# Performance work log

Hardware: AMD Instinct MI355X
Metric: run time of the kernel (lower is better)

Reference implementation:

```python
import jax, jax.numpy as jnp
import numpy as np

D_MODEL = 1024
N_HEADS = 16
HEAD_DIM = D_MODEL // N_HEADS
B, S = 2, 2048


def setup_inputs() -> dict:
    key = jax.random.key(0)
    ks = jax.random.split(key, 12)
    std = 1.0 / np.sqrt(D_MODEL)
    mk = lambda k: (jax.random.normal(k, (D_MODEL, D_MODEL), jnp.float32) * std)
    return {
        "query": jax.random.normal(ks[0], (B, S, D_MODEL), jnp.float32),
        "key": jax.random.normal(ks[1], (B, S, D_MODEL), jnp.float32),
        "value": jax.random.normal(ks[2], (B, S, D_MODEL), jnp.float32),
        "Wq": mk(ks[3]), "bq": jnp.zeros((D_MODEL,), jnp.float32),
        "Wk": mk(ks[4]), "bk": jnp.zeros((D_MODEL,), jnp.float32),
        "Wv": mk(ks[5]), "bv": jnp.zeros((D_MODEL,), jnp.float32),
        "Wo": mk(ks[6]), "bo": jnp.zeros((D_MODEL,), jnp.float32),
    }


def reference(query, key, value, Wq, bq, Wk, bk, Wv, bv, Wo, bo):
    b, s, d = query.shape
    # Linear projections (torch Linear: x @ W.T + b)
    q = query @ Wq.T + bq
    k = key @ Wk.T + bk
    v = value @ Wv.T + bv
    # [B, H, S, Dh]
    split = lambda x: x.reshape(b, -1, N_HEADS, HEAD_DIM).transpose(0, 2, 1, 3)
    qh, kh, vh = split(q), split(k), split(v)
    scores = jnp.einsum("bhqd,bhkd->bhqk", qh, kh) / jnp.sqrt(
        jnp.asarray(HEAD_DIM, qh.dtype))
    attn = jax.nn.softmax(scores, axis=-1)
    out = jnp.einsum("bhqk,bhkd->bhqd", attn, vh)
    out = out.transpose(0, 2, 1, 3).reshape(b, -1, N_HEADS * HEAD_DIM)
    return out @ Wo.T + bo
```

## Files before the change

kernel.cpp:

```cpp
#include <hip/hip_runtime.h>
#include <hip/hip_bf16.h>


typedef short bf16x8 __attribute__((ext_vector_type(8)));
typedef short bf16x4 __attribute__((ext_vector_type(4)));
typedef float f32x4  __attribute__((ext_vector_type(4)));

constexpr size_t NE = (size_t)4096 * 1024;
constexpr size_t NW = (size_t)1024 * 1024;

#if __has_builtin(__builtin_amdgcn_exp2f)
#define EXP2(x) __builtin_amdgcn_exp2f(x)
#else
#define EXP2(x) exp2f(x)
#endif

__device__ __forceinline__ short f2bf(float f) {
  __hip_bfloat16 h = __float2bfloat16(f);
  return *reinterpret_cast<short*>(&h);
}

__device__ __forceinline__ void cp16(const short* g, short* l) {
  __builtin_amdgcn_global_load_lds(
      (const __attribute__((address_space(1))) void*)g,
      (__attribute__((address_space(3))) void*)l, 16, 0, 0);
}

__device__ __forceinline__ int xcd_swz(int x, int nblk) {
  return (x & 7) * (nblk >> 3) + (x >> 3);
}

__global__ __launch_bounds__(256) void cvt_kernel(
    const float* q, const float* k, const float* v,
    const float* Wq, const float* Wk, const float* Wv, const float* Wo,
    short* qb, short* kb, short* vb,
    short* Wqb, short* Wkb, short* Wvb, short* Wob) {
  const int y = blockIdx.y;
  const float* s; short* d;
  if (y < 12) {
    const int t = y >> 2;
    const size_t off = (size_t)(y & 3) << 20;
    s = (t == 0 ? q : (t == 1 ? k : v)) + off;
    d = (t == 0 ? qb : (t == 1 ? kb : vb)) + off;
  } else {
    s = (y == 12 ? Wq : (y == 13 ? Wk : (y == 14 ? Wv : Wo)));
    d = (y == 12 ? Wqb : (y == 13 ? Wkb : (y == 14 ? Wvb : Wob)));
  }
  size_t i = (size_t)blockIdx.x * 256 + threadIdx.x;
  float4 val = ((const float4*)s)[i];
  bf16x4 o;
  o[0] = f2bf(val.x); o[1] = f2bf(val.y); o[2] = f2bf(val.z); o[3] = f2bf(val.w);
  ((bf16x4*)d)[i] = o;
}

__global__ __launch_bounds__(256) void gemm_qkv(
    const short* __restrict__ A0, const short* __restrict__ A1, const short* __restrict__ A2,
    const short* __restrict__ W0, const short* __restrict__ W1, const short* __restrict__ W2,
    const float* __restrict__ b0, const float* __restrict__ b1, const float* __restrict__ b2,
    short* __restrict__ C0, short* __restrict__ C1, short* __restrict__ Cv) {
  __shared__ short As[3][128 * 32];
  __shared__ short Bs[3][128 * 32];
  const int which = blockIdx.y;
  const short* A    = which == 0 ? A0 : (which == 1 ? A1 : A2);
  const short* W    = which == 0 ? W0 : (which == 1 ? W1 : W2);
  const float* bias = which == 0 ? b0 : (which == 1 ? b1 : b2);
  const float scale = which == 0 ? 0.18033688011112042f : 1.0f;

  const int tid  = threadIdx.x;
  const int bx   = xcd_swz((int)blockIdx.x, 256);
  const int bm   = bx >> 3;
  const int bn   = bx & 7;
  const int lane = tid & 63, wid = tid >> 6;
  const int g = lane >> 4, l15 = lane & 15;
  const int wm = (wid >> 1) * 64, wn = (wid & 1) * 64;

  const short* Ag = A + (size_t)(bm * 128 + (tid >> 2)) * 1024 + (tid & 3) * 8;
  const short* Wg = W + (size_t)(bn * 128 + (tid >> 2)) * 1024 + (tid & 3) * 8;
  const int wofs = wid * 512;

#define QKV_STAGE(t, b)                               \
  do {                                                \
    const int kk_ = (t) * 32;                         \
    cp16(Ag + kk_,             As[(b)] + wofs);       \
    cp16(Ag + 64 * 1024 + kk_, As[(b)] + wofs + 2048);\
    cp16(Wg + kk_,             Bs[(b)] + wofs);       \
    cp16(Wg + 64 * 1024 + kk_, Bs[(b)] + wofs + 2048);\
  } while (0)

  f32x4 acc[4][4];
#pragma unroll
  for (int i = 0; i < 4; ++i)
#pragma unroll
    for (int j = 0; j < 4; ++j) acc[i][j] = (f32x4){0.f, 0.f, 0.f, 0.f};

  QKV_STAGE(0, 0);
  QKV_STAGE(1, 1);

  for (int t = 0; t < 32; ++t) {
    const int cur = t % 3;
    if (t < 30) {
      QKV_STAGE(t + 2, (t + 2) % 3);
      asm volatile("s_waitcnt vmcnt(8)" ::: "memory");
    } else if (t == 30) {
      asm volatile("s_waitcnt vmcnt(4)" ::: "memory");
    } else {
      asm volatile("s_waitcnt vmcnt(0)" ::: "memory");
    }
    __builtin_amdgcn_s_barrier();

    bf16x8 af[4], bfr[4];
#pragma unroll
    for (int mt = 0; mt < 4; ++mt)
      af[mt] = *(const bf16x8*)&As[cur][(wm + mt * 16 + l15) * 32 + g * 8];
#pragma unroll
    for (int nt = 0; nt < 4; ++nt)
      bfr[nt] = *(const bf16x8*)&Bs[cur][(wn + nt * 16 + l15) * 32 + g * 8];
#pragma unroll
    for (int mt = 0; mt < 4; ++mt)
#pragma unroll
      for (int nt = 0; nt < 4; ++nt)
        acc[mt][nt] = __builtin_amdgcn_mfma_f32_16x16x32_bf16(
            af[mt], bfr[nt], acc[mt][nt], 0, 0, 0);

    asm volatile("s_waitcnt lgkmcnt(0)" ::: "memory");
    __builtin_amdgcn_s_barrier();
  }
#undef QKV_STAGE

  const int col0 = bn * 128 + wn;
  if (which < 2) {
    short* C = which == 0 ? C0 : C1;
#pragma unroll
    for (int nt = 0; nt < 4; ++nt) {
      const int col = col0 + nt * 16 + l15;
      const float bb = bias[col];
#pragma unroll
      for (int mt = 0; mt < 4; ++mt) {
        const int m0 = bm * 128 + wm + mt * 16 + g * 4;
#pragma unroll
        for (int r = 0; r < 4; ++r)
          C[(size_t)(m0 + r) * 1024 + col] = f2bf((acc[mt][nt][r] + bb) * scale);
      }
    }
  } else {
#pragma unroll
    for (int nt = 0; nt < 4; ++nt) {
      const int col = col0 + nt * 16 + l15;
      const int h = col >> 6, dh = col & 63;
      const float bb = bias[col];
#pragma unroll
      for (int mt = 0; mt < 4; ++mt) {
        const int m0 = bm * 128 + wm + mt * 16 + g * 4;
        const int bb_ = m0 >> 11, s0 = m0 & 2047;
        bf16x4 o;
#pragma unroll
        for (int r = 0; r < 4; ++r) o[r] = f2bf(acc[mt][nt][r] + bb);
        *(bf16x4*)&Cv[(((size_t)bb_ * 16 + h) * 64 + dh) * 2048 + s0] = o;
      }
    }
  }
}

__global__ __launch_bounds__(256) void gemm_out(
    const short* __restrict__ A, const short* __restrict__ W,
    const float* __restrict__ bias, float* __restrict__ C) {
  __shared__ short As[3][64 * 32];
  __shared__ short Bs[3][128 * 32];
  const int tid  = threadIdx.x;
  const int bx   = xcd_swz((int)blockIdx.x, 512);
  const int bm   = bx >> 3;
  const int bn   = bx & 7;
  const int lane = tid & 63, wid = tid >> 6;
  const int g = lane >> 4, l15 = lane & 15;
  const int wm = (wid >> 1) * 32, wn = (wid & 1) * 64;

  const short* Ag = A + (size_t)(bm * 64 + (tid >> 2)) * 1024 + (tid & 3) * 8;
  const short* Wg = W + (size_t)(bn * 128 + (tid >> 2)) * 1024 + (tid & 3) * 8;
  const int wofs = wid * 512;

#define OUT_STAGE(t, b)                               \
  do {                                                \
    const int kk_ = (t) * 32;                         \
    cp16(Ag + kk_,             As[(b)] + wofs);       \
    cp16(Wg + kk_,             Bs[(b)] + wofs);       \
    cp16(Wg + 64 * 1024 + kk_, Bs[(b)] + wofs + 2048);\
  } while (0)

  f32x4 acc[2][4];
#pragma unroll
  for (int i = 0; i < 2; ++i)
#pragma unroll
    for (int j = 0; j < 4; ++j) acc[i][j] = (f32x4){0.f, 0.f, 0.f, 0.f};

  OUT_STAGE(0, 0);
  OUT_STAGE(1, 1);

  for (int t = 0; t < 32; ++t) {
    const int cur = t % 3;
    if (t < 30) {
      OUT_STAGE(t + 2, (t + 2) % 3);
      asm volatile("s_waitcnt vmcnt(6)" ::: "memory");
    } else if (t == 30) {
      asm volatile("s_waitcnt vmcnt(3)" ::: "memory");
    } else {
      asm volatile("s_waitcnt vmcnt(0)" ::: "memory");
    }
    __builtin_amdgcn_s_barrier();

    bf16x8 af[2], bfr[4];
#pragma unroll
    for (int mt = 0; mt < 2; ++mt)
      af[mt] = *(const bf16x8*)&As[cur][(wm + mt * 16 + l15) * 32 + g * 8];
#pragma unroll
    for (int nt = 0; nt < 4; ++nt)
      bfr[nt] = *(const bf16x8*)&Bs[cur][(wn + nt * 16 + l15) * 32 + g * 8];
#pragma unroll
    for (int mt = 0; mt < 2; ++mt)
#pragma unroll
      for (int nt = 0; nt < 4; ++nt)
        acc[mt][nt] = __builtin_amdgcn_mfma_f32_16x16x32_bf16(
            af[mt], bfr[nt], acc[mt][nt], 0, 0, 0);

    asm volatile("s_waitcnt lgkmcnt(0)" ::: "memory");
    __builtin_amdgcn_s_barrier();
  }
#undef OUT_STAGE

  const int col0 = bn * 128 + wn;
#pragma unroll
  for (int nt = 0; nt < 4; ++nt) {
    const int col = col0 + nt * 16 + l15;
    const float bb = bias[col];
#pragma unroll
    for (int mt = 0; mt < 2; ++mt) {
      const int m0 = bm * 64 + wm + mt * 16 + g * 4;
#pragma unroll
      for (int r = 0; r < 4; ++r)
        C[(size_t)(m0 + r) * 1024 + col] = acc[mt][nt][r] + bb;
    }
  }
}

__global__ __launch_bounds__(512) void attn_kernel(
    const short* __restrict__ Q, const short* __restrict__ K,
    const short* __restrict__ Vg, short* __restrict__ O) {
  __shared__ __align__(16) char smem[73728];
  short (*Kt)[64][72] = (short(*)[64][72])smem;
  short (*Vt)[64][72] = (short(*)[64][72])(smem + 18432);
  short (*Pt)[32][72] = (short(*)[32][72])(smem + 36864);
  float* M = (float*)smem;

  const int tid  = threadIdx.x;
  const int bx   = xcd_swz((int)blockIdx.x, 512);
  const int qt   = bx & 15;
  const int bh   = bx >> 4;
  const int b    = bh >> 4, h = bh & 15;
  const int lane = tid & 63, wid = tid >> 6;
  const int par  = wid >> 2;
  const int w4   = wid & 3;
  const int g = lane >> 4, l15 = lane & 15;

  const int q0 = qt * 128 + w4 * 32;
  bf16x8 qf[2][2];
#pragma unroll
  for (int mt = 0; mt < 2; ++mt) {
    const size_t base = (size_t)(b * 2048 + q0 + mt * 16 + l15) * 1024 + h * 64;
    qf[mt][0] = *(const bf16x8*)(Q + base + g * 8);
    qf[mt][1] = *(const bf16x8*)(Q + base + 32 + g * 8);
  }

  f32x4 o_acc[2][4];
#pragma unroll
  for (int i = 0; i < 2; ++i)
#pragma unroll
    for (int j = 0; j < 4; ++j) o_acc[i][j] = (f32x4){0.f, 0.f, 0.f, 0.f};
  float l_i[2][4];
#pragma unroll
  for (int i = 0; i < 2; ++i)
#pragma unroll
    for (int r = 0; r < 4; ++r) l_i[i][r] = 0.f;

  const int st   = tid & 255;
  const int spar = tid >> 8;
  const int srow = st >> 2, sch = st & 3;
  const short* Kbase = K + (size_t)(b * 2048) * 1024 + h * 64 + sch * 8;
  const short* Vbase = Vg + (size_t)((b * 16 + h) * 64 + srow) * 2048 + sch * 8;

  bf16x8 nk0, nk1, nv0, nv1;
  {
    const short* krow = Kbase + (size_t)(spar * 64 + srow) * 1024;
    nk0 = *(const bf16x8*)(krow);
    nk1 = *(const bf16x8*)(krow + 32);
    nv0 = *(const bf16x8*)(Vbase + spar * 64);
    nv1 = *(const bf16x8*)(Vbase + spar * 64 + 32);
  }

  for (int ktp = 0; ktp < 16; ++ktp) {
    __syncthreads();
    *(bf16x8*)&Kt[spar][srow][sch * 8]      = nk0;
    *(bf16x8*)&Kt[spar][srow][sch * 8 + 32] = nk1;
    *(bf16x8*)&Vt[spar][srow][sch * 8]      = nv0;
    *(bf16x8*)&Vt[spar][srow][sch * 8 + 32] = nv1;
    __syncthreads();

    if (ktp < 15) {
      const int kn = (ktp + 1) * 2 + spar;
      const short* krow = Kbase + (size_t)(kn * 64 + srow) * 1024;
      nk0 = *(const bf16x8*)(krow);
      nk1 = *(const bf16x8*)(krow + 32);
      nv0 = *(const bf16x8*)(Vbase + kn * 64);
      nv1 = *(const bf16x8*)(Vbase + kn * 64 + 32);
    }

    f32x4 sv[2][4];
#pragma unroll
    for (int nt = 0; nt < 4; ++nt) {
      bf16x8 kf0 = *(const bf16x8*)&Kt[par][nt * 16 + l15][g * 8];
      bf16x8 kf1 = *(const bf16x8*)&Kt[par][nt * 16 + l15][32 + g * 8];
#pragma unroll
      for (int mt = 0; mt < 2; ++mt) {
        f32x4 z = (f32x4){0.f, 0.f, 0.f, 0.f};
        z = __builtin_amdgcn_mfma_f32_16x16x32_bf16(qf[mt][0], kf0, z, 0, 0, 0);
        z = __builtin_amdgcn_mfma_f32_16x16x32_bf16(qf[mt][1], kf1, z, 0, 0, 0);
        sv[mt][nt] = z;
      }
    }

#pragma unroll
    for (int mt = 0; mt < 2; ++mt)
#pragma unroll
      for (int r = 0; r < 4; ++r) {
        float p0 = EXP2(sv[mt][0][r]);
        float p1 = EXP2(sv[mt][1][r]);
        float p2 = EXP2(sv[mt][2][r]);
        float p3 = EXP2(sv[mt][3][r]);
        l_i[mt][r] += (p0 + p1) + (p2 + p3);
        const int pr = mt * 16 + g * 4 + r;
        Pt[wid][pr][l15]      = f2bf(p0);
        Pt[wid][pr][16 + l15] = f2bf(p1);
        Pt[wid][pr][32 + l15] = f2bf(p2);
        Pt[wid][pr][48 + l15] = f2bf(p3);
      }

    bf16x8 pf[2][2];
#pragma unroll
    for (int mt = 0; mt < 2; ++mt) {
      pf[mt][0] = *(const bf16x8*)&Pt[wid][mt * 16 + l15][g * 8];
      pf[mt][1] = *(const bf16x8*)&Pt[wid][mt * 16 + l15][32 + g * 8];
    }
#pragma unroll
    for (int nt = 0; nt < 4; ++nt) {
      bf16x8 vf0 = *(const bf16x8*)&Vt[par][nt * 16 + l15][g * 8];
      bf16x8 vf1 = *(const bf16x8*)&Vt[par][nt * 16 + l15][32 + g * 8];
#pragma unroll
      for (int mt = 0; mt < 2; ++mt) {
        o_acc[mt][nt] = __builtin_amdgcn_mfma_f32_16x16x32_bf16(
            pf[mt][0], vf0, o_acc[mt][nt], 0, 0, 0);
        o_acc[mt][nt] = __builtin_amdgcn_mfma_f32_16x16x32_bf16(
            pf[mt][1], vf1, o_acc[mt][nt], 0, 0, 0);
      }
    }
  }

  __syncthreads();
  if (par == 1) {
    float* dst = M + (size_t)(w4 * 64 + lane) * 40;
#pragma unroll
    for (int mt = 0; mt < 2; ++mt)
#pragma unroll
      for (int nt = 0; nt < 4; ++nt)
        *(f32x4*)(dst + (mt * 4 + nt) * 4) = o_acc[mt][nt];
#pragma unroll
    for (int mt = 0; mt < 2; ++mt)
#pragma unroll
      for (int r = 0; r < 4; ++r) dst[32 + mt * 4 + r] = l_i[mt][r];
  }
  __syncthreads();
  if (par == 0) {
    const float* src = M + (size_t)(w4 * 64 + lane) * 40;
#pragma unroll
    for (int mt = 0; mt < 2; ++mt)
#pragma unroll
      for (int nt = 0; nt < 4; ++nt)
        o_acc[mt][nt] += *(const f32x4*)(src + (mt * 4 + nt) * 4);
#pragma unroll
    for (int mt = 0; mt < 2; ++mt)
#pragma unroll
      for (int r = 0; r < 4; ++r) l_i[mt][r] += src[32 + mt * 4 + r];

#pragma unroll
    for (int mt = 0; mt < 2; ++mt)
#pragma unroll
      for (int r = 0; r < 4; ++r) {
        float l = l_i[mt][r];
#pragma unroll
        for (int off = 1; off < 16; off <<= 1) l += __shfl_xor(l, off, 64);
        const float inv = 1.0f / l;
        const int row = q0 + mt * 16 + g * 4 + r;
        const size_t base = (size_t)(b * 2048 + row) * 1024 + h * 64;
#pragma unroll
        for (int nt = 0; nt < 4; ++nt)
          O[base + nt * 16 + l15] = f2bf(o_acc[mt][nt][r] * inv);
      }
  }
}

extern "C" void kernel_launch(void* const* d_in, const int* in_sizes, int n_in,
                              void* d_out, int out_size, void* d_ws, size_t ws_size,
                              hipStream_t stream) {
  (void)in_sizes; (void)n_in; (void)out_size; (void)ws_size;
  const float* q  = (const float*)d_in[0];
  const float* k  = (const float*)d_in[1];
  const float* v  = (const float*)d_in[2];
  const float* Wq = (const float*)d_in[3];
  const float* bq = (const float*)d_in[4];
  const float* Wk = (const float*)d_in[5];
  const float* bk = (const float*)d_in[6];
  const float* Wv = (const float*)d_in[7];
  const float* bv = (const float*)d_in[8];
  const float* Wo = (const float*)d_in[9];
  const float* bo = (const float*)d_in[10];
  float* out = (float*)d_out;

  short* qb  = (short*)d_ws;
  short* kb  = qb + NE;
  short* vb  = kb + NE;
  short* Wqb = vb + NE;
  short* Wkb = Wqb + NW;
  short* Wvb = Wkb + NW;
  short* Wob = Wvb + NW;
  short* Qw  = Wob + NW;
  short* Kw  = Qw + NE;
  short* Vtg = Kw + NE;
  short* Ob  = qb;

  cvt_kernel<<<dim3(1024, 16), 256, 0, stream>>>(q, k, v, Wq, Wk, Wv, Wo,
                                                 qb, kb, vb, Wqb, Wkb, Wvb, Wob);
  gemm_qkv<<<dim3(256, 3), 256, 0, stream>>>(qb, kb, vb, Wqb, Wkb, Wvb,
                                             bq, bk, bv, Qw, Kw, Vtg);
  attn_kernel<<<512, 512, 0, stream>>>(Qw, Kw, Vtg, Ob);
  gemm_out<<<512, 256, 0, stream>>>(Ob, Wob, bo, out);
}
```

Measured before the change: 219.1 us.

## Keep attention P in registers via transposed MFMA and permuted V layout

Swaps the MFMA operand order so the score tile comes out transposed (keys along rows), letting the exp'd probabilities be packed directly into the B-operand registers for the PV MFMA instead of round-tripping through LDS. To make this work, the V projection epilogue writes sequence positions in a permuted order within each 64-chunk so the register layout matches. This removes the P LDS buffer, halving shared memory and adding an occupancy hint, and the row-sum and output store become simpler (fewer shuffles, vectorized bf16x4 stores). It relies on the permutation exactly matching the MFMA fragment layout, so any mismatch would silently corrupt results.

New measurement: 321.1 us. 1.47x slower.

```diff
diff --git a/kernel.cpp b/kernel.cpp
--- a/kernel.cpp
+++ b/kernel.cpp
@@ -152,10 +152,13 @@
       for (int mt = 0; mt < 4; ++mt) {
         const int m0 = bm * 128 + wm + mt * 16 + g * 4;
         const int bb_ = m0 >> 11, s0 = m0 & 2047;
+        const int k6 = s0 & 63;
+        const int cpos = (s0 & ~63) | (((k6 >> 4) & 2) << 4)
+                       | (((k6 >> 2) & 3) << 3) | (((k6 >> 4) & 1) << 2);
         bf16x4 o;
 #pragma unroll
         for (int r = 0; r < 4; ++r) o[r] = f2bf(acc[mt][nt][r] + bb);
-        *(bf16x4*)&Cv[(((size_t)bb_ * 16 + h) * 64 + dh) * 2048 + s0] = o;
+        *(bf16x4*)&Cv[(((size_t)bb_ * 16 + h) * 64 + dh) * 2048 + cpos] = o;
       }
     }
   }
@@ -241,13 +244,12 @@
   }
 }
 
-__global__ __launch_bounds__(512) void attn_kernel(
+__global__ __launch_bounds__(512, 6) void attn_kernel(
     const short* __restrict__ Q, const short* __restrict__ K,
     const short* __restrict__ Vg, short* __restrict__ O) {
-  __shared__ __align__(16) char smem[73728];
+  __shared__ __align__(16) char smem[36864];
   short (*Kt)[64][72] = (short(*)[64][72])smem;
   short (*Vt)[64][72] = (short(*)[64][72])(smem + 18432);
-  short (*Pt)[32][72] = (short(*)[32][72])(smem + 36864);
   float* M = (float*)smem;
 
   const int tid  = threadIdx.x;
@@ -274,11 +276,7 @@
   for (int i = 0; i < 2; ++i)
 #pragma unroll
     for (int j = 0; j < 4; ++j) o_acc[i][j] = (f32x4){0.f, 0.f, 0.f, 0.f};
-  float l_i[2][4];
-#pragma unroll
-  for (int i = 0; i < 2; ++i)
-#pragma unroll
-    for (int r = 0; r < 4; ++r) l_i[i][r] = 0.f;
+  float l_i[2] = {0.f, 0.f};
 
   const int st   = tid & 255;
   const int spar = tid >> 8;
@@ -320,34 +318,27 @@
 #pragma unroll
       for (int mt = 0; mt < 2; ++mt) {
         f32x4 z = (f32x4){0.f, 0.f, 0.f, 0.f};
-        z = __builtin_amdgcn_mfma_f32_16x16x32_bf16(qf[mt][0], kf0, z, 0, 0, 0);
-        z = __builtin_amdgcn_mfma_f32_16x16x32_bf16(qf[mt][1], kf1, z, 0, 0, 0);
+        z = __builtin_amdgcn_mfma_f32_16x16x32_bf16(kf0, qf[mt][0], z, 0, 0, 0);
+        z = __builtin_amdgcn_mfma_f32_16x16x32_bf16(kf1, qf[mt][1], z, 0, 0, 0);
         sv[mt][nt] = z;
       }
     }
 
-#pragma unroll
-    for (int mt = 0; mt < 2; ++mt)
-#pragma unroll
-      for (int r = 0; r < 4; ++r) {
-        float p0 = EXP2(sv[mt][0][r]);
-        float p1 = EXP2(sv[mt][1][r]);
-        float p2 = EXP2(sv[mt][2][r]);
-        float p3 = EXP2(sv[mt][3][r]);
-        l_i[mt][r] += (p0 + p1) + (p2 + p3);
-        const int pr = mt * 16 + g * 4 + r;
-        Pt[wid][pr][l15]      = f2bf(p0);
-        Pt[wid][pr][16 + l15] = f2bf(p1);
-        Pt[wid][pr][32 + l15] = f2bf(p2);
-        Pt[wid][pr][48 + l15] = f2bf(p3);
-      }
-
     bf16x8 pf[2][2];
 #pragma unroll
     for (int mt = 0; mt < 2; ++mt) {
-      pf[mt][0] = *(const bf16x8*)&Pt[wid][mt * 16 + l15][g * 8];
-      pf[mt][1] = *(const bf16x8*)&Pt[wid][mt * 16 + l15][32 + g * 8];
-    }
+      float s = 0.f;
+#pragma unroll
+      for (int nt = 0; nt < 4; ++nt)
+#pragma unroll
+        for (int r = 0; r < 4; ++r) {
+          float p = EXP2(sv[mt][nt][r]);
+          s += p;
+          pf[mt][nt >> 1][(nt & 1) * 4 + r] = f2bf(p);
+        }
+      l_i[mt] += s;
+    }
+
 #pragma unroll
     for (int nt = 0; nt < 4; ++nt) {
       bf16x8 vf0 = *(const bf16x8*)&Vt[par][nt * 16 + l15][g * 8];
@@ -355,53 +346,51 @@
 #pragma unroll
       for (int mt = 0; mt < 2; ++mt) {
         o_acc[mt][nt] = __builtin_amdgcn_mfma_f32_16x16x32_bf16(
-            pf[mt][0], vf0, o_acc[mt][nt], 0, 0, 0);
+            vf0, pf[mt][0], o_acc[mt][nt], 0, 0, 0);
         o_acc[mt][nt] = __builtin_amdgcn_mfma_f32_16x16x32_bf16(
-            pf[mt][1], vf1, o_acc[mt][nt], 0, 0, 0);
+            vf1, pf[mt][1], o_acc[mt][nt], 0, 0, 0);
       }
     }
   }
 
   __syncthreads();
   if (par == 1) {
-    float* dst = M + (size_t)(w4 * 64 + lane) * 40;
+    float* dst = M + (size_t)(w4 * 64 + lane) * 36;
 #pragma unroll
     for (int mt = 0; mt < 2; ++mt)
 #pragma unroll
       for (int nt = 0; nt < 4; ++nt)
         *(f32x4*)(dst + (mt * 4 + nt) * 4) = o_acc[mt][nt];
-#pragma unroll
-    for (int mt = 0; mt < 2; ++mt)
-#pragma unroll
-      for (int r = 0; r < 4; ++r) dst[32 + mt * 4 + r] = l_i[mt][r];
+    dst[32] = l_i[0];
+    dst[33] = l_i[1];
   }
   __syncthreads();
   if (par == 0) {
-    const float* src = M + (size_t)(w4 * 64 + lane) * 40;
+    const float* src = M + (size_t)(w4 * 64 + lane) * 36;
 #pragma unroll
     for (int mt = 0; mt < 2; ++mt)
 #pragma unroll
       for (int nt = 0; nt < 4; ++nt)
         o_acc[mt][nt] += *(const f32x4*)(src + (mt * 4 + nt) * 4);
-#pragma unroll
-    for (int mt = 0; mt < 2; ++mt)
-#pragma unroll
-      for (int r = 0; r < 4; ++r) l_i[mt][r] += src[32 + mt * 4 + r];
-
-#pragma unroll
-    for (int mt = 0; mt < 2; ++mt)
-#pragma unroll
-      for (int r = 0; r < 4; ++r) {
-        float l = l_i[mt][r];
-#pragma unroll
-        for (int off = 1; off < 16; off <<= 1) l += __shfl_xor(l, off, 64);
-        const float inv = 1.0f / l;
-        const int row = q0 + mt * 16 + g * 4 + r;
-        const size_t base = (size_t)(b * 2048 + row) * 1024 + h * 64;
-#pragma unroll
-        for (int nt = 0; nt < 4; ++nt)
-          O[base + nt * 16 + l15] = f2bf(o_acc[mt][nt][r] * inv);
+    l_i[0] += src[32];
+    l_i[1] += src[33];
+
+#pragma unroll
+    for (int mt = 0; mt < 2; ++mt) {
+      float l = l_i[mt];
+      l += __shfl_xor(l, 16, 64);
+      l += __shfl_xor(l, 32, 64);
+      const float inv = 1.0f / l;
+      const int row = q0 + mt * 16 + l15;
+      const size_t base = (size_t)(b * 2048 + row) * 1024 + h * 64;
+#pragma unroll
+      for (int nt = 0; nt < 4; ++nt) {
+        bf16x4 o;
+#pragma unroll
+        for (int r = 0; r < 4; ++r) o[r] = f2bf(o_acc[mt][nt][r] * inv);
+        *(bf16x4*)&O[base + nt * 16 + g * 4] = o;
       }
+    }
   }
 }
 
```
